# Performance work log

Hardware: AMD Instinct MI355X
Metric: run time of the kernel (lower is better)

Reference implementation:

```python
import jax, jax.numpy as jnp
import numpy as np

N = 50000
E = 800000
IN_CH = 128
HID = 64
HEADS = 2
OUT_CH = 5
NEG_SLOPE = 0.2


def glorot(key, shape):
    fan_in, fan_out = shape[0], shape[-1]
    lim = jnp.sqrt(6.0 / (fan_in + fan_out))
    return jax.random.uniform(key, shape, jnp.float32, -lim, lim)


def setup_inputs() -> dict:
    key = jax.random.key(0)
    ks = jax.random.split(key, 20)
    x = jax.random.normal(ks[0], (N, IN_CH), jnp.float32)
    edge_index = jax.random.randint(ks[1], (2, E), 0, N, jnp.int32)
    edge_attr = jax.random.uniform(ks[2], (E, 1), jnp.float32)
    # layer 1: in=128 -> heads=2, out=64 (concat)
    W1l = glorot(ks[3], (IN_CH, HEADS * HID)); b1l = jnp.zeros((HEADS * HID,), jnp.float32)
    W1r = glorot(ks[4], (IN_CH, HEADS * HID)); b1r = jnp.zeros((HEADS * HID,), jnp.float32)
    W1e = glorot(ks[5], (1, HEADS * HID)); b1e = jnp.zeros((HEADS * HID,), jnp.float32)
    att1 = glorot(ks[6], (HEADS, HID))
    bias1 = jnp.zeros((HEADS * HID,), jnp.float32)
    # layer 2: in=128 -> heads=1, out=5
    W2l = glorot(ks[7], (HEADS * HID, OUT_CH)); b2l = jnp.zeros((OUT_CH,), jnp.float32)
    W2r = glorot(ks[8], (HEADS * HID, OUT_CH)); b2r = jnp.zeros((OUT_CH,), jnp.float32)
    W2e = glorot(ks[9], (1, OUT_CH)); b2e = jnp.zeros((OUT_CH,), jnp.float32)
    att2 = glorot(ks[10], (1, OUT_CH))
    bias2 = jnp.zeros((OUT_CH,), jnp.float32)
    return dict(x=x, edge_index=edge_index, edge_attr=edge_attr,
                W1l=W1l, b1l=b1l, W1r=W1r, b1r=b1r, W1e=W1e, b1e=b1e, att1=att1, bias1=bias1,
                W2l=W2l, b2l=b2l, W2r=W2r, b2r=b2r, W2e=W2e, b2e=b2e, att2=att2, bias2=bias2)


def gatv2_layer(x, src, dst, edge_attr, Wl, bl, Wr, br, We, be, att, bias, heads, out_ch, concat):
    n = x.shape[0]
    xl = (x @ Wl + bl).reshape(n, heads, out_ch)   # source transform
    xr = (x @ Wr + br).reshape(n, heads, out_ch)   # target transform
    ee = (edge_attr @ We + be).reshape(-1, heads, out_ch)
    # GATv2 score: a^T LeakyReLU(xl[src] + xr[dst] + e)
    s = xl[src] + xr[dst] + ee                      # [E, H, C]
    s = jnp.where(s > 0, s, NEG_SLOPE * s)
    logits = jnp.einsum('ehc,hc->eh', s, att)       # [E, H]
    # segment softmax over incoming edges of each destination node
    mx = jax.ops.segment_max(logits, dst, num_segments=n)
    ex = jnp.exp(logits - mx[dst])
    den = jax.ops.segment_sum(ex, dst, num_segments=n)
    alpha = ex / den[dst]                           # [E, H]
    msg = alpha[:, :, None] * xl[src]               # [E, H, C]
    out = jax.ops.segment_sum(msg, dst, num_segments=n)  # [N, H, C]
    if concat:
        out = out.reshape(n, heads * out_ch)
    else:
        out = out.mean(axis=1)
    return out + bias


def reference(x, edge_index, edge_attr,
              W1l, b1l, W1r, b1r, W1e, b1e, att1, bias1,
              W2l, b2l, W2r, b2r, W2e, b2e, att2, bias2):
    src, dst = edge_index[0], edge_index[1]
    h = gatv2_layer(x, src, dst, edge_attr, W1l, b1l, W1r, b1r, W1e, b1e, att1, bias1,
                    HEADS, HID, True)
    h = jax.nn.elu(h)
    out = gatv2_layer(h, src, dst, edge_attr, W2l, b2l, W2r, b2r, W2e, b2e, att2, bias2,
                      1, OUT_CH, True)
    return out
```

## Files before the change

### kernel.cpp

```cpp
#include <hip/hip_runtime.h>
#include <hip/hip_bf16.h>
#include <math.h>

#define NN 50000
#define NE 800000
#define NZB 3125
#define CAP 48
#define NEG_SLOPE 0.2f
#define LOG2E 1.44269504088896340736f
#define EPT 4
#define NSB 782
#define NGB 3125

typedef __attribute__((ext_vector_type(8))) short bf16x8;
typedef __attribute__((ext_vector_type(4))) float f32x4;
typedef __attribute__((ext_vector_type(2))) float f32x2;


__device__ __forceinline__ float ldf(const void* p, long i, int isbf) {
    if (isbf) {
        unsigned short raw = ((const unsigned short*)p)[i];
        return __uint_as_float(((unsigned)raw) << 16);
    }
    return ((const float*)p)[i];
}

__device__ __forceinline__ short f2bs(float f) {
    __hip_bfloat16 h = __float2bfloat16(f);
    short s; __builtin_memcpy(&s, &h, 2); return s;
}
__device__ __forceinline__ unsigned short f2bu(float f) {
    __hip_bfloat16 h = __float2bfloat16(f);
    unsigned short s; __builtin_memcpy(&s, &h, 2); return s;
}

__device__ __forceinline__ float red16(float p) {
    p += __int_as_float(__builtin_amdgcn_update_dpp(
             0, __float_as_int(p), 0xB1, 0xF, 0xF, false));
    p += __int_as_float(__builtin_amdgcn_update_dpp(
             0, __float_as_int(p), 0x4E, 0xF, 0xF, false));
    p += __int_as_float(__builtin_amdgcn_update_dpp(
             0, __float_as_int(p), 0x141, 0xF, 0xF, false));
    p += __int_as_float(__builtin_amdgcn_update_dpp(
             0, __float_as_int(p), 0x140, 0xF, 0xF, false));
    return p;
}

__device__ __forceinline__ float red32(float p) {
    p = red16(p);
    p += __int_as_float(__builtin_amdgcn_ds_swizzle(__float_as_int(p), 0x401F));
    return p;
}

__global__ void k_setup_wprep(const void* x, int* flag, unsigned* cnt,
                              const void* __restrict__ Wl,
                              const void* __restrict__ Wr,
                              unsigned short* __restrict__ bfrag,
                              const void* __restrict__ W1e,
                              const void* __restrict__ att1,
                              const void* __restrict__ bias1,
                              const void* __restrict__ W2l,
                              const void* __restrict__ b2l,
                              const void* __restrict__ W2r,
                              const void* __restrict__ b2r,
                              const void* __restrict__ b2e,
                              const void* __restrict__ W2e,
                              const void* __restrict__ att2,
                              const void* __restrict__ bias2,
                              float* __restrict__ prm) {
    if (blockIdx.x < NZB) {
        int i = blockIdx.x * 256 + threadIdx.x;
        if (i < NN * 16) cnt[i] = 0u;
        return;
    }
    unsigned short raw0 = ((const unsigned short*)x)[(threadIdx.x & 63) * 2];
    float v0 = __uint_as_float(((unsigned)raw0) << 16);
    bool sane = isfinite(v0) && fabsf(v0) > 1e-5f && fabsf(v0) < 1e3f;
    const int isbf = (__popcll(__ballot(sane)) > 32) ? 1 : 0;
    if (blockIdx.x == NZB && threadIdx.x == 0) *flag = isbf;
    if (blockIdx.x == NZB + 128) {
        const int t = threadIdx.x;
        if (t < 128) {
            prm[t]       = ldf(W1e, t, isbf);
            prm[128 + t] = ldf(att1, t, isbf) * LOG2E;
            prm[256 + t] = ldf(bias1, t, isbf);
#pragma unroll
            for (int c = 0; c < 5; c++) {
                prm[384 + c * 128 + t]  = ldf(W2l, (long)t * 5 + c, isbf);
                prm[1024 + c * 128 + t] = ldf(W2r, (long)t * 5 + c, isbf);
            }
        } else if (t < 133) {
            const int c = t - 128;
            prm[1664 + c] = ldf(b2l, c, isbf);
            prm[1669 + c] = ldf(b2r, c, isbf) + ldf(b2e, c, isbf);
            prm[1674 + c] = ldf(W2e, c, isbf);
            prm[1679 + c] = ldf(att2, c, isbf) * LOG2E;
            prm[1684 + c] = ldf(bias2, c, isbf);
        }
        return;
    }
    int idx = (blockIdx.x - NZB) * 256 + threadIdx.x;
    int j = idx & 7, lane = (idx >> 3) & 63, ks = (idx >> 9) & 3, nt = idx >> 11;
    int k = ks * 32 + (lane >> 4) * 8 + j;
    int n = nt * 16 + (lane & 15);
    float v = (n < 128) ? ldf(Wl, (long)k * 128 + n, isbf)
                        : ldf(Wr, (long)k * 128 + (n - 128), isbf);
    bfrag[idx] = f2bu(v);
}

__global__ __launch_bounds__(256) void k_lin1_scatter(
    const void* __restrict__ x, const unsigned short* __restrict__ bfrag,
    const void* __restrict__ bl, const void* __restrict__ br,
    const void* __restrict__ be1,
    unsigned short* __restrict__ xl, unsigned short* __restrict__ xr,
    const int* __restrict__ ei, const void* __restrict__ ea,
    unsigned* __restrict__ cnt, unsigned* __restrict__ sedge,
    const int* __restrict__ flag) {
    const int isbf = flag[0];
    if (blockIdx.x < NSB) {
        const int e0 = blockIdx.x * (256 * EPT) + threadIdx.x;
        int dv[EPT], sv[EPT];
        float avv[EPT];
        unsigned pos[EPT];
#pragma unroll
        for (int k = 0; k < EPT; k++) {
            const int e = e0 + k * 256;
            if (e < NE) {
                dv[k] = ei[NE + e];
                sv[k] = ei[e];
                avv[k] = ldf(ea, e, isbf);
            } else dv[k] = -1;
        }
#pragma unroll
        for (int k = 0; k < EPT; k++)
            if (dv[k] >= 0)
                pos[k] = atomicAdd(&cnt[(long)dv[k] * 16], 1u);
#pragma unroll
        for (int k = 0; k < EPT; k++)
            if (dv[k] >= 0 && pos[k] < CAP)
                sedge[(long)dv[k] * CAP + pos[k]] =
                    (__float_as_uint(avv[k]) & 0xffff0000u) | (unsigned)sv[k];
        return;
    }
    const int wave = threadIdx.x >> 6, lane = threadIdx.x & 63;
    const int mrow = lane & 15, quad = lane >> 4;
    const long mbase = (long)(blockIdx.x - NSB) * 16;
    bf16x8 afrag[4];
    if (isbf) {
        const unsigned short* xp = (const unsigned short*)x
                                 + (mbase + mrow) * 128 + quad * 8;
#pragma unroll
        for (int ks = 0; ks < 4; ks++)
            afrag[ks] = *(const bf16x8*)(xp + ks * 32);
    } else {
        const float* xp = (const float*)x + (mbase + mrow) * 128 + quad * 8;
#pragma unroll
        for (int ks = 0; ks < 4; ks++) {
            const float4 u0 = *(const float4*)(xp + ks * 32);
            const float4 u1 = *(const float4*)(xp + ks * 32 + 4);
            bf16x8 a;
            a[0] = f2bs(u0.x); a[1] = f2bs(u0.y); a[2] = f2bs(u0.z); a[3] = f2bs(u0.w);
            a[4] = f2bs(u1.x); a[5] = f2bs(u1.y); a[6] = f2bs(u1.z); a[7] = f2bs(u1.w);
            afrag[ks] = a;
        }
    }
#pragma unroll
    for (int q = 0; q < 4; q++) {
        const int nt = wave * 4 + q;
        f32x4 acc = {0.f, 0.f, 0.f, 0.f};
#pragma unroll
        for (int ks = 0; ks < 4; ks++) {
            const bf16x8 bfr = *(const bf16x8*)(bfrag + ((nt * 4 + ks) * 64 + lane) * 8);
            acc = __builtin_amdgcn_mfma_f32_16x16x32_bf16(afrag[ks], bfr, acc, 0, 0, 0);
        }
        const int ng = nt * 16 + (lane & 15);
        const float bv = (ng < 128)
            ? ldf(bl, ng, isbf)
            : ldf(br, ng - 128, isbf) + ldf(be1, ng - 128, isbf);
        unsigned short* dst = (ng < 128) ? xl : xr;
        const int col = ng & 127;
#pragma unroll
        for (int reg = 0; reg < 4; reg++) {
            const long row = mbase + quad * 4 + reg;
            dst[row * 128 + col] = f2bu(acc[reg] + bv);
        }
    }
}

__device__ __forceinline__ void edge1(unsigned eg, const unsigned* __restrict__ xl,
                                      int lane, f32x2 wev, f32x2 xrv, f32x2 atv,
                                      float& lsum, f32x2& accv) {
    const int s = (int)(eg & 0xffffu);
    const float e = __uint_as_float(eg & 0xffff0000u);
    const unsigned* row = xl + ((long)s << 6);
    const unsigned rw = row[lane];
    f32x2 xv;
    xv.x = __uint_as_float(rw << 16);
    xv.y = __uint_as_float(rw & 0xffff0000u);
    f32x2 t = xv + __builtin_elementwise_fma((f32x2){e, e}, wev, xrv);
    t = __builtin_elementwise_max(t, t * (f32x2){NEG_SLOPE, NEG_SLOPE});
    const f32x2 pd = t * atv;
    float p = red32(pd.x + pd.y);
    p = fminf(fmaxf(p, -60.f), 60.f);
    const float w = __builtin_amdgcn_exp2f(p);
    lsum += w;
    accv = __builtin_elementwise_fma((f32x2){w, w}, xv, accv);
}

__global__ __launch_bounds__(256) void k_attn1(
    const unsigned* __restrict__ deg, const unsigned* __restrict__ sedge,
    const unsigned* __restrict__ xl, const unsigned* __restrict__ xr,
    const float* __restrict__ prm,
    unsigned short* __restrict__ xl2b, float* __restrict__ xr2) {
    const int n = __builtin_amdgcn_readfirstlane(
        blockIdx.x * 4 + (threadIdx.x >> 6));
    if (n >= NN) return;
    const int lane = threadIdx.x & 63;
    const unsigned rraw = xr[(long)n * 64 + lane];
    const f32x2 xrv = {__uint_as_float(rraw << 16),
                       __uint_as_float(rraw & 0xffff0000u)};
    const float2 wet = *(const float2*)(prm + 2 * lane);
    const f32x2 wev = {wet.x, wet.y};
    const float2 att_ = *(const float2*)(prm + 128 + 2 * lane);
    const f32x2 atv = {att_.x, att_.y};
    float lsum0 = 0.f, lsum1 = 0.f, lsum2 = 0.f, lsum3 = 0.f;
    f32x2 accv0 = {0.f, 0.f}, accv1 = {0.f, 0.f};
    f32x2 accv2 = {0.f, 0.f}, accv3 = {0.f, 0.f};
    const int dg = min((int)__builtin_amdgcn_readfirstlane(deg[(long)n * 16]), CAP);
    const long base = (long)n * CAP;
    const uint4* __restrict__ sld = (const uint4*)(sedge + base);
    const int dg4 = dg & ~3;
    int g = 0;
    if (dg4 > 0) {
        uint4 eg4 = sld[0];
        for (g = 0; g < dg4; g += 4) {
            uint4 nxt = eg4;
            if (g + 4 < dg4) nxt = sld[(g >> 2) + 1];
            edge1(eg4.x, xl, lane, wev, xrv, atv, lsum0, accv0);
            edge1(eg4.y, xl, lane, wev, xrv, atv, lsum1, accv1);
            edge1(eg4.z, xl, lane, wev, xrv, atv, lsum2, accv2);
            edge1(eg4.w, xl, lane, wev, xrv, atv, lsum3, accv3);
            eg4 = nxt;
        }
    }
    for (; g < dg; ++g)
        edge1(sedge[base + g], xl, lane, wev, xrv, atv, lsum0, accv0);
    const float l = (lsum0 + lsum1) + (lsum2 + lsum3);
    const f32x2 av = (accv0 + accv1) + (accv2 + accv3);
    const float inv = 1.f / fmaxf(l, 1e-20f);
    const float2 bsv = *(const float2*)(prm + 256 + 2 * lane);
    float h0 = fmaf(av.x, inv, bsv.x);
    float h1 = fmaf(av.y, inv, bsv.y);
    h0 = h0 > 0.f ? h0 : __builtin_amdgcn_exp2f(h0 * LOG2E) - 1.f;
    h1 = h1 > 0.f ? h1 : __builtin_amdgcn_exp2f(h1 * LOG2E) - 1.f;
    float pl[5], pr[5];
#pragma unroll
    for (int c = 0; c < 5; c++) {
        const float2 wl = *(const float2*)(prm + 384 + c * 128 + 2 * lane);
        const float2 wr = *(const float2*)(prm + 1024 + c * 128 + 2 * lane);
        pl[c] = h0 * wl.x + h1 * wl.y;
        pr[c] = h0 * wr.x + h1 * wr.y;
        pl[c] = red16(pl[c]);
        pr[c] = red16(pr[c]);
    }
#pragma unroll
    for (int off = 16; off <= 32; off <<= 1) {
#pragma unroll
        for (int c = 0; c < 5; c++) {
            pl[c] += __shfl_xor(pl[c], off);
            pr[c] += __shfl_xor(pr[c], off);
        }
    }
    if (lane == 0) {
        uint4 pk;
        pk.x = (unsigned)f2bu(pl[0] + prm[1664])
             | ((unsigned)f2bu(pl[1] + prm[1665]) << 16);
        pk.y = (unsigned)f2bu(pl[2] + prm[1666])
             | ((unsigned)f2bu(pl[3] + prm[1667]) << 16);
        pk.z = (unsigned)f2bu(pl[4] + prm[1668]);
        pk.w = 0u;
        *(uint4*)(xl2b + (long)n * 8) = pk;
#pragma unroll
        for (int c = 0; c < 5; c++)
            xr2[(long)n * 8 + c] = pr[c] + prm[1669 + c];
    }
}

__global__ __launch_bounds__(256) void k_attn2(
    const unsigned* __restrict__ deg, const unsigned* __restrict__ sedge,
    const unsigned short* __restrict__ xl2b, const float* __restrict__ xr2,
    const float* __restrict__ prm,
    void* __restrict__ out, const int* __restrict__ flag) {
    const int isbf = flag[0];
    const int n = blockIdx.x * 16 + (threadIdx.x >> 4);
    if (n >= NN) return;
    const int l16 = threadIdx.x & 15;
    f32x4 xrb4; float xrb4s;
    f32x4 wev4; float wev4s;
    f32x4 atv4; float atv4s;
    {
        const float4 r0 = *(const float4*)(xr2 + (long)n * 8);
        xrb4 = (f32x4){r0.x, r0.y, r0.z, r0.w};
        xrb4s = xr2[(long)n * 8 + 4];
        wev4 = (f32x4){prm[1674], prm[1675], prm[1676], prm[1677]};
        wev4s = prm[1678];
        atv4 = (f32x4){prm[1679], prm[1680], prm[1681], prm[1682]};
        atv4s = prm[1683];
    }
    const f32x4 ns4 = {NEG_SLOPE, NEG_SLOPE, NEG_SLOPE, NEG_SLOPE};
    float lw = 0.f, laccs = 0.f;
    f32x4 lacc4 = {0.f, 0.f, 0.f, 0.f};
    const int dg = min((int)deg[(long)n * 16], CAP);
    const long base = (long)n * CAP;
    for (int idx = l16; idx < dg; idx += 16) {
        const unsigned eg = sedge[base + idx];
        const int s = eg & 0xffffu;
        const float a = __uint_as_float(eg & 0xffff0000u);
        const uint4 u = *(const uint4*)(xl2b + (long)s * 8);
        f32x4 xls4;
        xls4.x = __uint_as_float(u.x << 16);
        xls4.y = __uint_as_float(u.x & 0xffff0000u);
        xls4.z = __uint_as_float(u.y << 16);
        xls4.w = __uint_as_float(u.y & 0xffff0000u);
        const float xlss = __uint_as_float(u.z << 16);
        f32x4 v4 = xls4 + __builtin_elementwise_fma((f32x4){a, a, a, a}, wev4, xrb4);
        v4 = __builtin_elementwise_max(v4, v4 * ns4);
        float vs = xlss + fmaf(a, wev4s, xrb4s);
        vs = fmaxf(vs, NEG_SLOPE * vs);
        const f32x4 pd = v4 * atv4;
        float p = ((pd.x + pd.y) + (pd.z + pd.w)) + vs * atv4s;
        p = fminf(fmaxf(p, -60.f), 60.f);
        const float w = __builtin_amdgcn_exp2f(p);
        lw += w;
        lacc4 = __builtin_elementwise_fma((f32x4){w, w, w, w}, xls4, lacc4);
        laccs = fmaf(w, xlss, laccs);
    }
    lw = red16(lw);
    lacc4.x = red16(lacc4.x);
    lacc4.y = red16(lacc4.y);
    lacc4.z = red16(lacc4.z);
    lacc4.w = red16(lacc4.w);
    laccs = red16(laccs);
    if (l16 == 0) {
        const float inv = 1.f / fmaxf(lw, 1e-20f);
        float o[5] = {lacc4.x, lacc4.y, lacc4.z, lacc4.w, laccs};
#pragma unroll
        for (int c = 0; c < 5; c++) {
            const float v = fmaf(o[c], inv, prm[1684 + c]);
            if (isbf) ((__hip_bfloat16*)out)[(long)n * 5 + c] = __float2bfloat16(v);
            else      ((float*)out)[(long)n * 5 + c] = v;
        }
    }
}

extern "C" void kernel_launch(void* const* d_in, const int* in_sizes, int n_in,
                              void* d_out, int out_size, void* d_ws, size_t ws_size,
                              hipStream_t stream) {
    const void* x    = d_in[0];
    const int*  ei   = (const int*)d_in[1];
    const void* ea   = d_in[2];
    const void* W1l  = d_in[3];
    const void* b1l  = d_in[4];
    const void* W1r  = d_in[5];
    const void* b1r  = d_in[6];
    const void* W1e  = d_in[7];
    const void* b1e  = d_in[8];
    const void* att1 = d_in[9];
    const void* bias1= d_in[10];
    const void* W2l  = d_in[11];
    const void* b2l  = d_in[12];
    const void* W2r  = d_in[13];
    const void* b2r  = d_in[14];
    const void* W2e  = d_in[15];
    const void* b2e  = d_in[16];
    const void* att2 = d_in[17];
    const void* bias2= d_in[18];

    float* W = (float*)d_ws;
    int*            flag    = (int*)W;
    float*          prm     = W + 110000;
    unsigned*       sedge   = (unsigned*)(W + 120000);
    unsigned*       cnt     = (unsigned*)(W + 2520000);
    unsigned short* xl1b    = (unsigned short*)(W + 3400000);
    unsigned short* xr1b    = (unsigned short*)(W + 6600000);
    unsigned short* bfrag   = (unsigned short*)(W + 9800000);
    unsigned short* xl2b    = (unsigned short*)(W + 9900000);
    float*          xr2     = W + 10300000;

    k_setup_wprep<<<NZB + 129, 256, 0, stream>>>(x, flag, cnt, W1l, W1r, bfrag,
                                                 W1e, att1, bias1,
                                                 W2l, b2l, W2r, b2r, b2e,
                                                 W2e, att2, bias2, prm);
    k_lin1_scatter<<<NSB + NGB, 256, 0, stream>>>(
        x, bfrag, b1l, b1r, b1e, xl1b, xr1b, ei, ea, cnt, sedge, flag);
    k_attn1<<<(NN + 3) / 4, 256, 0, stream>>>(cnt, sedge,
                                              (const unsigned*)xl1b, (const unsigned*)xr1b,
                                              prm, xl2b, xr2);
    k_attn2<<<(NN * 16 + 255) / 256, 256, 0, stream>>>(cnt, sedge, xl2b, xr2,
                                                       prm, d_out, flag);
}
```

Before: 228.9 us.

## Replace per-destination global atomics with two-pass coarse bucket edge partitioning

Edge bucketing is split into two passes. The first pass builds a block-local shared-memory histogram over 49 coarse destination ranges and claims space in each coarse bucket with one global atomic per bucket. A new kernel then rescans each coarse bucket eight times, once per 128-node slice, and places edges with LDS atomics, writing a compact per-node degree array. This removes the 3125-block zeroing of the padded counter array and the 800k scattered global atomics, at the cost of an extra launch, a coarse staging buffer that aliases the layer-2 outputs, repeated reads of each coarse bucket, and silently dropped edges if a bucket exceeds CCAP.

```diff
diff --git a/kernel.cpp b/kernel.cpp
--- a/kernel.cpp
+++ b/kernel.cpp
@@ -4,13 +4,14 @@
 
 #define NN 50000
 #define NE 800000
-#define NZB 3125
 #define CAP 48
 #define NEG_SLOPE 0.2f
 #define LOG2E 1.44269504088896340736f
-#define EPT 4
-#define NSB 782
+#define NPB 782
 #define NGB 3125
+#define NCB 49
+#define CCAP 17408
+#define QPB 8
 
 typedef __attribute__((ext_vector_type(8))) short bf16x8;
 typedef __attribute__((ext_vector_type(4))) float f32x4;
@@ -52,7 +53,7 @@
     return p;
 }
 
-__global__ void k_setup_wprep(const void* x, int* flag, unsigned* cnt,
+__global__ void k_setup_wprep(const void* x, int* flag, unsigned* gcnt,
                               const void* __restrict__ Wl,
                               const void* __restrict__ Wr,
                               unsigned short* __restrict__ bfrag,
@@ -68,18 +69,14 @@
                               const void* __restrict__ att2,
                               const void* __restrict__ bias2,
                               float* __restrict__ prm) {
-    if (blockIdx.x < NZB) {
-        int i = blockIdx.x * 256 + threadIdx.x;
-        if (i < NN * 16) cnt[i] = 0u;
-        return;
-    }
     unsigned short raw0 = ((const unsigned short*)x)[(threadIdx.x & 63) * 2];
     float v0 = __uint_as_float(((unsigned)raw0) << 16);
     bool sane = isfinite(v0) && fabsf(v0) > 1e-5f && fabsf(v0) < 1e3f;
     const int isbf = (__popcll(__ballot(sane)) > 32) ? 1 : 0;
-    if (blockIdx.x == NZB && threadIdx.x == 0) *flag = isbf;
-    if (blockIdx.x == NZB + 128) {
+    if (blockIdx.x == 128) {
         const int t = threadIdx.x;
+        if (t == 0) *flag = isbf;
+        if (t >= 192 && t < 192 + NCB) gcnt[t - 192] = 0u;
         if (t < 128) {
             prm[t]       = ldf(W1e, t, isbf);
             prm[128 + t] = ldf(att1, t, isbf) * LOG2E;
@@ -99,7 +96,7 @@
         }
         return;
     }
-    int idx = (blockIdx.x - NZB) * 256 + threadIdx.x;
+    int idx = blockIdx.x * 256 + threadIdx.x;
     int j = idx & 7, lane = (idx >> 3) & 63, ks = (idx >> 9) & 3, nt = idx >> 11;
     int k = ks * 32 + (lane >> 4) * 8 + j;
     int n = nt * 16 + (lane & 15);
@@ -108,43 +105,62 @@
     bfrag[idx] = f2bu(v);
 }
 
-__global__ __launch_bounds__(256) void k_lin1_scatter(
+__global__ __launch_bounds__(256) void k_part1_lin1(
     const void* __restrict__ x, const unsigned short* __restrict__ bfrag,
     const void* __restrict__ bl, const void* __restrict__ br,
     const void* __restrict__ be1,
     unsigned short* __restrict__ xl, unsigned short* __restrict__ xr,
     const int* __restrict__ ei, const void* __restrict__ ea,
-    unsigned* __restrict__ cnt, unsigned* __restrict__ sedge,
+    unsigned* __restrict__ gcnt, uint2* __restrict__ coarse,
     const int* __restrict__ flag) {
     const int isbf = flag[0];
-    if (blockIdx.x < NSB) {
-        const int e0 = blockIdx.x * (256 * EPT) + threadIdx.x;
-        int dv[EPT], sv[EPT];
-        float avv[EPT];
-        unsigned pos[EPT];
-#pragma unroll
-        for (int k = 0; k < EPT; k++) {
+    if (blockIdx.x < NPB) {
+        __shared__ unsigned hist[64];
+        __shared__ unsigned base[64];
+        const int tid = threadIdx.x;
+        if (tid < 64) hist[tid] = 0u;
+        __syncthreads();
+        const int e0 = blockIdx.x * 1024 + tid;
+        int dv[4], sv[4];
+        float av[4];
+        unsigned lr[4];
+#pragma unroll
+        for (int k = 0; k < 4; k++) {
             const int e = e0 + k * 256;
             if (e < NE) {
                 dv[k] = ei[NE + e];
                 sv[k] = ei[e];
-                avv[k] = ldf(ea, e, isbf);
+                av[k] = ldf(ea, e, isbf);
             } else dv[k] = -1;
         }
 #pragma unroll
-        for (int k = 0; k < EPT; k++)
+        for (int k = 0; k < 4; k++)
             if (dv[k] >= 0)
-                pos[k] = atomicAdd(&cnt[(long)dv[k] * 16], 1u);
-#pragma unroll
-        for (int k = 0; k < EPT; k++)
-            if (dv[k] >= 0 && pos[k] < CAP)
-                sedge[(long)dv[k] * CAP + pos[k]] =
-                    (__float_as_uint(avv[k]) & 0xffff0000u) | (unsigned)sv[k];
+                lr[k] = atomicAdd(&hist[dv[k] >> 10], 1u);
+        __syncthreads();
+        if (tid < 64) {
+            const unsigned h = hist[tid];
+            base[tid] = h ? atomicAdd(&gcnt[tid], h) : 0u;
+        }
+        __syncthreads();
+#pragma unroll
+        for (int k = 0; k < 4; k++) {
+            if (dv[k] >= 0) {
+                const int cb = dv[k] >> 10;
+                const unsigned p = base[cb] + lr[k];
+                if (p < CCAP) {
+                    uint2 pay;
+                    pay.x = (__float_as_uint(av[k]) & 0xffff0000u) | (unsigned)sv[k];
+                    pay.y = (unsigned)dv[k];
+                    coarse[(long)cb * CCAP + p] = pay;
+                }
+            }
+        }
         return;
     }
     const int wave = threadIdx.x >> 6, lane = threadIdx.x & 63;
     const int mrow = lane & 15, quad = lane >> 4;
-    const long mbase = (long)(blockIdx.x - NSB) * 16;
+    const long mbase = (long)(blockIdx.x - NPB) * 16;
     bf16x8 afrag[4];
     if (isbf) {
         const unsigned short* xp = (const unsigned short*)x
@@ -184,6 +200,33 @@
             const long row = mbase + quad * 4 + reg;
             dst[row * 128 + col] = f2bu(acc[reg] + bv);
         }
+    }
+}
+
+__global__ __launch_bounds__(256) void k_part2(
+    const uint2* __restrict__ coarse, const unsigned* __restrict__ gcnt,
+    unsigned* __restrict__ sedge, unsigned* __restrict__ deg) {
+    const int cb = blockIdx.x >> 3, q = blockIdx.x & 7;
+    const int d0 = cb * 1024 + q * 128;
+    __shared__ unsigned lcnt[128];
+    const int tid = threadIdx.x;
+    if (tid < 128) lcnt[tid] = 0u;
+    __syncthreads();
+    const int m = min((int)gcnt[cb], CCAP);
+    const uint2* __restrict__ cbp = coarse + (long)cb * CCAP;
+    for (int i = tid; i < m; i += 256) {
+        const uint2 pay = cbp[i];
+        const int ld = (int)pay.y - d0;
+        if ((unsigned)ld < 128u) {
+            const unsigned pos = atomicAdd(&lcnt[ld], 1u);
+            if (pos < CAP)
+                sedge[(long)pay.y * CAP + pos] = pay.x;
+        }
+    }
+    __syncthreads();
+    if (tid < 128) {
+        const int d = d0 + tid;
+        if (d < NN) deg[d] = min(lcnt[tid], (unsigned)CAP);
     }
 }
 
@@ -226,7 +269,7 @@
     float lsum0 = 0.f, lsum1 = 0.f, lsum2 = 0.f, lsum3 = 0.f;
     f32x2 accv0 = {0.f, 0.f}, accv1 = {0.f, 0.f};
     f32x2 accv2 = {0.f, 0.f}, accv3 = {0.f, 0.f};
-    const int dg = min((int)__builtin_amdgcn_readfirstlane(deg[(long)n * 16]), CAP);
+    const int dg = (int)__builtin_amdgcn_readfirstlane(deg[n]);
     const long base = (long)n * CAP;
     const uint4* __restrict__ sld = (const uint4*)(sedge + base);
     const int dg4 = dg & ~3;
@@ -310,7 +353,7 @@
     const f32x4 ns4 = {NEG_SLOPE, NEG_SLOPE, NEG_SLOPE, NEG_SLOPE};
     float lw = 0.f, laccs = 0.f;
     f32x4 lacc4 = {0.f, 0.f, 0.f, 0.f};
-    const int dg = min((int)deg[(long)n * 16], CAP);
+    const int dg = (int)deg[n];
     const long base = (long)n * CAP;
     for (int idx = l16; idx < dg; idx += 16) {
         const unsigned eg = sedge[base + idx];
@@ -378,24 +421,27 @@
 
     float* W = (float*)d_ws;
     int*            flag    = (int*)W;
+    unsigned*       gcnt    = (unsigned*)(W + 100000);
     float*          prm     = W + 110000;
     unsigned*       sedge   = (unsigned*)(W + 120000);
-    unsigned*       cnt     = (unsigned*)(W + 2520000);
+    unsigned*       deg     = (unsigned*)(W + 2520000);
     unsigned short* xl1b    = (unsigned short*)(W + 3400000);
     unsigned short* xr1b    = (unsigned short*)(W + 6600000);
     unsigned short* bfrag   = (unsigned short*)(W + 9800000);
+    uint2*          coarse  = (uint2*)(W + 9900000);
     unsigned short* xl2b    = (unsigned short*)(W + 9900000);
     float*          xr2     = W + 10300000;
 
-    k_setup_wprep<<<NZB + 129, 256, 0, stream>>>(x, flag, cnt, W1l, W1r, bfrag,
-                                                 W1e, att1, bias1,
-                                                 W2l, b2l, W2r, b2r, b2e,
-                                                 W2e, att2, bias2, prm);
-    k_lin1_scatter<<<NSB + NGB, 256, 0, stream>>>(
-        x, bfrag, b1l, b1r, b1e, xl1b, xr1b, ei, ea, cnt, sedge, flag);
-    k_attn1<<<(NN + 3) / 4, 256, 0, stream>>>(cnt, sedge,
+    k_setup_wprep<<<129, 256, 0, stream>>>(x, flag, gcnt, W1l, W1r, bfrag,
+                                           W1e, att1, bias1,
+                                           W2l, b2l, W2r, b2r, b2e,
+                                           W2e, att2, bias2, prm);
+    k_part1_lin1<<<NPB + NGB, 256, 0, stream>>>(
+        x, bfrag, b1l, b1r, b1e, xl1b, xr1b, ei, ea, gcnt, coarse, flag);
+    k_part2<<<NCB * QPB, 256, 0, stream>>>(coarse, gcnt, sedge, deg);
+    k_attn1<<<(NN + 3) / 4, 256, 0, stream>>>(deg, sedge,
                                               (const unsigned*)xl1b, (const unsigned*)xr1b,
                                               prm, xl2b, xr2);
-    k_attn2<<<(NN * 16 + 255) / 256, 256, 0, stream>>>(cnt, sedge, xl2b, xr2,
+    k_attn2<<<(NN * 16 + 255) / 256, 256, 0, stream>>>(deg, sedge, xl2b, xr2,
                                                        prm, d_out, flag);
 }
```

Result: faster. 224.3 us (-2.0%).
